# Kernel tuning notes

Measured on AMD Instinct MI355X. Metric: run time of the kernel, lower is better.

The kernel has to match this reference:

```python
import jax, jax.numpy as jnp
import numpy as np

BITWIDTH = 7
M, K, N = 32768, 1024, 1024  # tokens, in_features, out_features


def _clip8(x):
    return jnp.clip(x, -127, 127).astype(jnp.int8)


def _range_bits(x):
    # RangeEstimate: ceil(log2(max|x|)) as int, 0 if all-zero
    r = jnp.max(jnp.abs(x).astype(jnp.float32))
    bits = jnp.ceil(jnp.log2(jnp.maximum(r, 1.0)))
    return jnp.where(r == 0, 0, bits).astype(jnp.int32)


def _round_shift(x, shift):
    # RoundShift (stochastic-style bit-shift rounding); shift is a traced int32 >= 1
    p = jnp.left_shift(jnp.int32(1), shift)
    rt = jnp.floor_divide(x, p)
    prob = x - rt * p
    dec = jnp.floor_divide(prob, jnp.left_shift(jnp.int32(1), shift - 1))
    return _clip8(rt + dec)


def setup_inputs() -> dict:
    key = jax.random.key(0)
    k1, k2 = jax.random.split(key)
    act_in = jax.random.randint(k1, (M, K), -127, 128, dtype=jnp.int32).astype(jnp.int8)
    weight = jax.random.randint(k2, (N, K), -127, 128, dtype=jnp.int32).astype(jnp.int8)
    exp_in = jnp.int32(0)
    weight_exp = jnp.int32(-11)  # ceil(log2(xavier bound)) - 7 for 1024x1024
    return {"act_in": act_in, "weight": weight, "exp_in": exp_in, "weight_exp": weight_exp}


def reference(act_in, weight, exp_in, weight_exp):
    # int8 GEMM with int32 accumulation: [M,K] @ [K,N]
    acc = jnp.matmul(act_in.astype(jnp.int32), weight.T.astype(jnp.int32))
    # act_calc: range-estimate + conditional bit-shift requantize to int8
    bits = _range_bits(acc)
    shift = bits - BITWIDTH
    pos = shift > 0
    sc = jnp.maximum(shift, 1)  # safe shift for the untaken branch
    act_out = jnp.where(pos, _round_shift(acc, sc), acc.astype(jnp.int8))
    exp_out = jnp.where(pos, exp_in + weight_exp + shift, exp_in + weight_exp)
    return act_out, exp_out
```

## Files before the change

kernel.cpp:

```cpp
#include <hip/hip_runtime.h>
#include <stdint.h>


#define MM 32768
#define NN 1024
#define KK 1024
#define BM 256
#define BN 128
#define BK 64
#define NKT (KK / BK)
#define TSA (BM * BK)
#define TSB (BN * BK)

typedef __attribute__((ext_vector_type(4))) int i32x4;
typedef __attribute__((ext_vector_type(16))) int i32x16;

#define BARRIER() asm volatile("s_barrier" ::: "memory")

__device__ __forceinline__ int pack4(int a, int b, int c, int d) {
  return (int)((unsigned)(a & 0xff) | ((unsigned)(b & 0xff) << 8) |
               ((unsigned)(c & 0xff) << 16) | ((unsigned)(d & 0xff) << 24));
}

__global__ void k_init(unsigned* slot) {
  if (threadIdx.x == 0) *slot = 0u;
}

__global__ void k_pack(const int* __restrict__ src, int8_t* __restrict__ dst, int n) {
  long t = (long)blockIdx.x * blockDim.x + threadIdx.x;
  long stride = (long)gridDim.x * blockDim.x;
  for (long i = t * 16; i < (long)n; i += stride * 16) {
    const i32x4* s = (const i32x4*)(src + i);
    i32x4 a0 = s[0], a1 = s[1], a2 = s[2], a3 = s[3];
    i32x4 o;
    o[0] = pack4(a0[0], a0[1], a0[2], a0[3]);
    o[1] = pack4(a1[0], a1[1], a1[2], a1[3]);
    o[2] = pack4(a2[0], a2[1], a2[2], a2[3]);
    o[3] = pack4(a3[0], a3[1], a3[2], a3[3]);
    *(i32x4*)(dst + i) = o;
  }
}

__global__ __launch_bounds__(512, 2)
void k_gemm(const int8_t* __restrict__ A8, const int8_t* __restrict__ B8,
            int* __restrict__ out, unsigned* __restrict__ maxslot) {
  __shared__ int8_t As[3][TSA];
  __shared__ int8_t Bs[3][TSB];

  const int tid  = threadIdx.x;
  const int lane = tid & 63;
  const int w    = tid >> 6;
  const int wm   = w >> 1;
  const int wn   = w & 1;

  const int orig = blockIdx.x;
  const int wgid = ((orig & 7) << 7) + (orig >> 3);
  const int bn = wgid & 7;
  const int bm = wgid >> 3;
  const int m0 = bm * BM;
  const int n0 = bn * BN;

  i32x16 acc[2][2];
#pragma unroll
  for (int i = 0; i < 2; ++i)
#pragma unroll
    for (int j = 0; j < 2; ++j) acc[i][j] = 0;

  auto stage = [&](int buf, int kt) {
    const int k0 = kt * BK;
#pragma unroll
    for (int q = 0; q < 2; ++q) {
      const int p   = (w * 2 + q) * 1024 + lane * 16;
      const int row = p >> 6;
      const int col = (p & 63) ^ (((row >> 1) & 3) << 4);
      __builtin_amdgcn_global_load_lds(
          (const __attribute__((address_space(1))) void*)(A8 + (size_t)(m0 + row) * KK + k0 + col),
          (__attribute__((address_space(3))) void*)(&As[buf][(w * 2 + q) * 1024]),
          16, 0, 0);
    }
    {
      const int p   = w * 1024 + lane * 16;
      const int row = p >> 6;
      const int col = (p & 63) ^ (((row >> 1) & 3) << 4);
      __builtin_amdgcn_global_load_lds(
          (const __attribute__((address_space(1))) void*)(B8 + (size_t)(n0 + row) * KK + k0 + col),
          (__attribute__((address_space(3))) void*)(&Bs[buf][w * 1024]),
          16, 0, 0);
    }
  };

  auto compute = [&](int buf) {
#pragma unroll
    for (int ks = 0; ks < 2; ++ks) {
      i32x4 af[2], bf[2];
#pragma unroll
      for (int ni = 0; ni < 2; ++ni) {
        const int row = wn * 64 + ni * 32 + (lane & 31);
        const int a = row * BK +
            ((ks * 32 + ((lane >> 5) << 4)) ^ (((row >> 1) & 3) << 4));
        bf[ni] = *(const i32x4*)(&Bs[buf][a]);
      }
#pragma unroll
      for (int mi = 0; mi < 2; ++mi) {
        const int row = wm * 64 + mi * 32 + (lane & 31);
        const int a = row * BK +
            ((ks * 32 + ((lane >> 5) << 4)) ^ (((row >> 1) & 3) << 4));
        af[mi] = *(const i32x4*)(&As[buf][a]);
      }
      __builtin_amdgcn_s_setprio(1);
#pragma unroll
      for (int mi = 0; mi < 2; ++mi)
#pragma unroll
        for (int ni = 0; ni < 2; ++ni)
          acc[mi][ni] = __builtin_amdgcn_mfma_i32_32x32x32_i8(
              af[mi], bf[ni], acc[mi][ni], 0, 0, 0);
      __builtin_amdgcn_s_setprio(0);
    }
  };

  stage(0, 0);
  stage(1, 1);
  asm volatile("s_waitcnt vmcnt(3)" ::: "memory");
  BARRIER();

  int b0 = 0, b1 = 1, b2 = 2;
  for (int kt = 0; kt < NKT; ++kt) {
    const bool more2 = (kt + 2 < NKT);
    if (more2) stage(b2, kt + 2);
    compute(b0);
    if (kt + 1 < NKT) {
      if (more2) { asm volatile("s_waitcnt vmcnt(3)" ::: "memory"); }
      else       { asm volatile("s_waitcnt vmcnt(0)" ::: "memory"); }
      BARRIER();
    }
    const int t = b0; b0 = b1; b1 = b2; b2 = t;
  }

  int mx = 0;
#pragma unroll
  for (int mi = 0; mi < 2; ++mi)
#pragma unroll
    for (int ni = 0; ni < 2; ++ni)
#pragma unroll
      for (int rg = 0; rg < 16; ++rg) {
        int x = acc[mi][ni][rg];
        int a = x < 0 ? -x : x;
        mx = a > mx ? a : mx;
      }
#pragma unroll
  for (int off = 32; off >= 1; off >>= 1) {
    int o = __shfl_xor(mx, off);
    mx = o > mx ? o : mx;
  }
  if (lane == 0) atomicMax(maxslot, (unsigned)mx);

#pragma unroll
  for (int mi = 0; mi < 2; ++mi)
#pragma unroll
    for (int ni = 0; ni < 2; ++ni) {
      const int mbase = m0 + wm * 64 + mi * 32;
      const int ncol  = n0 + wn * 64 + ni * 32 + (lane & 31);
#pragma unroll
      for (int rg = 0; rg < 16; ++rg) {
        const int mrow = mbase + (rg & 3) + ((rg >> 2) << 3) + ((lane >> 5) << 2);
        out[(size_t)mrow * NN + ncol] = acc[mi][ni][rg];
      }
    }
}

__global__ __launch_bounds__(256, 2)
void k_gemm_fb(const int* __restrict__ A32, const int* __restrict__ B32,
               int* __restrict__ out, unsigned* __restrict__ maxslot) {
  __shared__ int8_t As[128 * 128];
  __shared__ int8_t Bs[128 * 128];
  const int tid = threadIdx.x, lane = tid & 63, w = tid >> 6;
  const int wr = w >> 1, wc = w & 1;
  const int bn = blockIdx.x & 7, bm = blockIdx.x >> 3;
  const int m0 = bm * 128, n0 = bn * 128;
  i32x16 acc[2][2];
#pragma unroll
  for (int i = 0; i < 2; ++i)
#pragma unroll
    for (int j = 0; j < 2; ++j) acc[i][j] = 0;
  for (int kt = 0; kt < 8; ++kt) {
    const int k0 = kt * 128;
    __syncthreads();
#pragma unroll
    for (int j = 0; j < 4; ++j) {
      const int fb = (j * 256 + tid) * 16;
      const int row = fb >> 7;
      const int swz = fb ^ ((row & 7) << 4);
      const int col = fb & 127;
      const int* sa = A32 + (size_t)(m0 + row) * KK + k0 + col;
      const int* sb = B32 + (size_t)(n0 + row) * KK + k0 + col;
      i32x4 av, bv;
#pragma unroll
      for (int t = 0; t < 4; ++t) {
        i32x4 ta = ((const i32x4*)sa)[t];
        i32x4 tb = ((const i32x4*)sb)[t];
        av[t] = pack4(ta[0], ta[1], ta[2], ta[3]);
        bv[t] = pack4(tb[0], tb[1], tb[2], tb[3]);
      }
      *(i32x4*)(As + swz) = av;
      *(i32x4*)(Bs + swz) = bv;
    }
    __syncthreads();
#pragma unroll
    for (int ks = 0; ks < 4; ++ks) {
      i32x4 af[2], bf[2];
#pragma unroll
      for (int mi = 0; mi < 2; ++mi) {
        const int row = wr * 64 + mi * 32 + (lane & 31);
        int a = row * 128 + ks * 32 + ((lane >> 5) << 4);
        a ^= (row & 7) << 4;
        af[mi] = *(const i32x4*)(As + a);
      }
#pragma unroll
      for (int ni = 0; ni < 2; ++ni) {
        const int row = wc * 64 + ni * 32 + (lane & 31);
        int a = row * 128 + ks * 32 + ((lane >> 5) << 4);
        a ^= (row & 7) << 4;
        bf[ni] = *(const i32x4*)(Bs + a);
      }
#pragma unroll
      for (int mi = 0; mi < 2; ++mi)
#pragma unroll
        for (int ni = 0; ni < 2; ++ni)
          acc[mi][ni] = __builtin_amdgcn_mfma_i32_32x32x32_i8(
              af[mi], bf[ni], acc[mi][ni], 0, 0, 0);
    }
  }
  int mx = 0;
#pragma unroll
  for (int mi = 0; mi < 2; ++mi)
#pragma unroll
    for (int ni = 0; ni < 2; ++ni)
#pragma unroll
      for (int rg = 0; rg < 16; ++rg) {
        int x = acc[mi][ni][rg];
        int a = x < 0 ? -x : x;
        mx = a > mx ? a : mx;
      }
#pragma unroll
  for (int off = 32; off >= 1; off >>= 1) {
    int o = __shfl_xor(mx, off);
    mx = o > mx ? o : mx;
  }
  if (lane == 0) atomicMax(maxslot, (unsigned)mx);
#pragma unroll
  for (int mi = 0; mi < 2; ++mi)
#pragma unroll
    for (int ni = 0; ni < 2; ++ni) {
      const int mbase = m0 + wr * 64 + mi * 32;
      const int ncol = n0 + wc * 64 + ni * 32 + (lane & 31);
#pragma unroll
      for (int rg = 0; rg < 16; ++rg) {
        const int mrow = mbase + (rg & 3) + ((rg >> 2) << 3) + ((lane >> 5) << 2);
        out[(size_t)mrow * NN + ncol] = acc[mi][ni][rg];
      }
    }
}

__global__ __launch_bounds__(256)
void k_requant(int* __restrict__ out, const unsigned* __restrict__ maxslot) {
  const unsigned r = *maxslot;
  const int bits  = (r <= 1u) ? 0 : (32 - __clz((int)(r - 1u)));
  const int shift = bits - 7;
  const size_t n = (size_t)MM * NN;
  size_t i = ((size_t)blockIdx.x * blockDim.x + threadIdx.x) * 4;
  const size_t stride = (size_t)gridDim.x * blockDim.x * 4;
  if (shift > 0) {
    for (; i < n; i += stride) {
      i32x4 v = *(i32x4*)(out + i);
#pragma unroll
      for (int j = 0; j < 4; ++j) {
        const int x = v[j];
        int t = (x >> shift) + ((x >> (shift - 1)) & 1);
        v[j] = t > 127 ? 127 : (t < -127 ? -127 : t);
      }
      *(i32x4*)(out + i) = v;
    }
  } else {
    for (; i < n; i += stride) {
      i32x4 v = *(i32x4*)(out + i);
#pragma unroll
      for (int j = 0; j < 4; ++j) v[j] = (int)(int8_t)v[j];
      *(i32x4*)(out + i) = v;
    }
  }
}

__global__ void k_final(int* __restrict__ out, const int* __restrict__ exp_in,
                        const int* __restrict__ wexp) {
  if (threadIdx.x == 0) {
    const unsigned r = *(const unsigned*)(out + (size_t)MM * NN);
    const int bits  = (r <= 1u) ? 0 : (32 - __clz((int)(r - 1u)));
    const int shift = bits - 7;
    out[(size_t)MM * NN] = *exp_in + *wexp + (shift > 0 ? shift : 0);
  }
}

extern "C" void kernel_launch(void* const* d_in, const int* in_sizes, int n_in,
                              void* d_out, int out_size, void* d_ws, size_t ws_size,
                              hipStream_t stream) {
  const int* act    = (const int*)d_in[0];
  const int* wgt    = (const int*)d_in[1];
  const int* exp_in = (const int*)d_in[2];
  const int* wexp   = (const int*)d_in[3];
  int* out          = (int*)d_out;
  unsigned* maxslot = (unsigned*)(out + (size_t)MM * NN);

  const size_t need = (size_t)(MM + NN) * KK + 256;

  k_init<<<1, 64, 0, stream>>>(maxslot);

  if (ws_size >= need) {
    int8_t* a8 = (int8_t*)d_ws;
    int8_t* w8 = a8 + (size_t)MM * KK;
    k_pack<<<2048, 256, 0, stream>>>(act, a8, MM * KK);
    k_pack<<<256, 256, 0, stream>>>(wgt, w8, NN * KK);
    const int grid = (MM / BM) * (NN / BN);
    k_gemm<<<grid, 512, 0, stream>>>(a8, w8, out, maxslot);
  } else {
    k_gemm_fb<<<(MM / 128) * (NN / 128), 256, 0, stream>>>(act, wgt, out, maxslot);
  }

  k_requant<<<4096, 256, 0, stream>>>(out, maxslot);
  k_final<<<1, 64, 0, stream>>>(out, exp_in, wexp);
}
```

Before: 195.9 us.

## Pack operands into MFMA fragment order and load directly from global

The pack kernel now writes int8 A and B in a pre-swizzled layout where each 1 KB block holds one 32x32 MFMA fragment, laid out in lane order. The GEMM then drops LDS staging, barriers and the triple buffer, and each wave loads its fragments straight from global memory with coalesced 16-byte loads. The block tile shrinks to 128x128 with 256 threads, which gives more blocks. This removes LDS traffic and sync costs, but A and B reuse now relies on L2 and there is no explicit prefetch pipeline, so global load latency may be exposed.

```diff
diff --git a/kernel.cpp b/kernel.cpp
--- a/kernel.cpp
+++ b/kernel.cpp
@@ -5,17 +5,9 @@
 #define MM 32768
 #define NN 1024
 #define KK 1024
-#define BM 256
-#define BN 128
-#define BK 64
-#define NKT (KK / BK)
-#define TSA (BM * BK)
-#define TSB (BN * BK)
 
 typedef __attribute__((ext_vector_type(4))) int i32x4;
 typedef __attribute__((ext_vector_type(16))) int i32x16;
-
-#define BARRIER() asm volatile("s_barrier" ::: "memory")
 
 __device__ __forceinline__ int pack4(int a, int b, int c, int d) {
   return (int)((unsigned)(a & 0xff) | ((unsigned)(b & 0xff) << 8) |
@@ -26,27 +18,30 @@
   if (threadIdx.x == 0) *slot = 0u;
 }
 
-__global__ void k_pack(const int* __restrict__ src, int8_t* __restrict__ dst, int n) {
-  long t = (long)blockIdx.x * blockDim.x + threadIdx.x;
-  long stride = (long)gridDim.x * blockDim.x;
-  for (long i = t * 16; i < (long)n; i += stride * 16) {
-    const i32x4* s = (const i32x4*)(src + i);
-    i32x4 a0 = s[0], a1 = s[1], a2 = s[2], a3 = s[3];
+__global__ void k_packf(const int* __restrict__ src, int8_t* __restrict__ dst,
+                        long nbytes) {
+  const long step = (long)gridDim.x * blockDim.x * 16;
+  for (long f = ((long)blockIdx.x * blockDim.x + threadIdx.x) * 16; f < nbytes;
+       f += step) {
+    const int tile = (int)(f >> 10);
+    const int lane = ((int)f >> 4) & 63;
+    const int mt = tile >> 5, kt2 = tile & 31;
+    const int row = mt * 32 + (lane & 31);
+    const int k   = kt2 * 32 + (lane >> 5) * 16;
+    const int* s = src + (size_t)row * KK + k;
     i32x4 o;
-    o[0] = pack4(a0[0], a0[1], a0[2], a0[3]);
-    o[1] = pack4(a1[0], a1[1], a1[2], a1[3]);
-    o[2] = pack4(a2[0], a2[1], a2[2], a2[3]);
-    o[3] = pack4(a3[0], a3[1], a3[2], a3[3]);
-    *(i32x4*)(dst + i) = o;
-  }
-}
-
-__global__ __launch_bounds__(512, 2)
-void k_gemm(const int8_t* __restrict__ A8, const int8_t* __restrict__ B8,
-            int* __restrict__ out, unsigned* __restrict__ maxslot) {
-  __shared__ int8_t As[3][TSA];
-  __shared__ int8_t Bs[3][TSB];
-
+#pragma unroll
+    for (int q = 0; q < 4; ++q) {
+      i32x4 t4 = ((const i32x4*)s)[q];
+      o[q] = pack4(t4[0], t4[1], t4[2], t4[3]);
+    }
+    *(i32x4*)(dst + f) = o;
+  }
+}
+
+__global__ __launch_bounds__(256)
+void k_gemmf(const int8_t* __restrict__ Af, const int8_t* __restrict__ Bf,
+             int* __restrict__ out, unsigned* __restrict__ maxslot) {
   const int tid  = threadIdx.x;
   const int lane = tid & 63;
   const int w    = tid >> 6;
@@ -54,11 +49,14 @@
   const int wn   = w & 1;
 
   const int orig = blockIdx.x;
-  const int wgid = ((orig & 7) << 7) + (orig >> 3);
+  const int wgid = ((orig & 7) << 8) + (orig >> 3);
   const int bn = wgid & 7;
   const int bm = wgid >> 3;
-  const int m0 = bm * BM;
-  const int n0 = bn * BN;
+
+  const int mtb = bm * 4 + wm * 2;
+  const int ntb = bn * 4 + wn * 2;
+  const int8_t* pa = Af + (size_t)mtb * 32 * 1024 + lane * 16;
+  const int8_t* pb = Bf + (size_t)ntb * 32 * 1024 + lane * 16;
 
   i32x16 acc[2][2];
 #pragma unroll
@@ -66,74 +64,17 @@
 #pragma unroll
     for (int j = 0; j < 2; ++j) acc[i][j] = 0;
 
-  auto stage = [&](int buf, int kt) {
-    const int k0 = kt * BK;
-#pragma unroll
-    for (int q = 0; q < 2; ++q) {
-      const int p   = (w * 2 + q) * 1024 + lane * 16;
-      const int row = p >> 6;
-      const int col = (p & 63) ^ (((row >> 1) & 3) << 4);
-      __builtin_amdgcn_global_load_lds(
-          (const __attribute__((address_space(1))) void*)(A8 + (size_t)(m0 + row) * KK + k0 + col),
-          (__attribute__((address_space(3))) void*)(&As[buf][(w * 2 + q) * 1024]),
-          16, 0, 0);
-    }
-    {
-      const int p   = w * 1024 + lane * 16;
-      const int row = p >> 6;
-      const int col = (p & 63) ^ (((row >> 1) & 3) << 4);
-      __builtin_amdgcn_global_load_lds(
-          (const __attribute__((address_space(1))) void*)(B8 + (size_t)(n0 + row) * KK + k0 + col),
-          (__attribute__((address_space(3))) void*)(&Bs[buf][w * 1024]),
-          16, 0, 0);
-    }
-  };
-
-  auto compute = [&](int buf) {
-#pragma unroll
-    for (int ks = 0; ks < 2; ++ks) {
-      i32x4 af[2], bf[2];
-#pragma unroll
-      for (int ni = 0; ni < 2; ++ni) {
-        const int row = wn * 64 + ni * 32 + (lane & 31);
-        const int a = row * BK +
-            ((ks * 32 + ((lane >> 5) << 4)) ^ (((row >> 1) & 3) << 4));
-        bf[ni] = *(const i32x4*)(&Bs[buf][a]);
-      }
-#pragma unroll
-      for (int mi = 0; mi < 2; ++mi) {
-        const int row = wm * 64 + mi * 32 + (lane & 31);
-        const int a = row * BK +
-            ((ks * 32 + ((lane >> 5) << 4)) ^ (((row >> 1) & 3) << 4));
-        af[mi] = *(const i32x4*)(&As[buf][a]);
-      }
-      __builtin_amdgcn_s_setprio(1);
-#pragma unroll
-      for (int mi = 0; mi < 2; ++mi)
-#pragma unroll
-        for (int ni = 0; ni < 2; ++ni)
-          acc[mi][ni] = __builtin_amdgcn_mfma_i32_32x32x32_i8(
-              af[mi], bf[ni], acc[mi][ni], 0, 0, 0);
-      __builtin_amdgcn_s_setprio(0);
-    }
-  };
-
-  stage(0, 0);
-  stage(1, 1);
-  asm volatile("s_waitcnt vmcnt(3)" ::: "memory");
-  BARRIER();
-
-  int b0 = 0, b1 = 1, b2 = 2;
-  for (int kt = 0; kt < NKT; ++kt) {
-    const bool more2 = (kt + 2 < NKT);
-    if (more2) stage(b2, kt + 2);
-    compute(b0);
-    if (kt + 1 < NKT) {
-      if (more2) { asm volatile("s_waitcnt vmcnt(3)" ::: "memory"); }
-      else       { asm volatile("s_waitcnt vmcnt(0)" ::: "memory"); }
-      BARRIER();
-    }
-    const int t = b0; b0 = b1; b1 = b2; b2 = t;
+#pragma unroll 4
+  for (int kt2 = 0; kt2 < 32; ++kt2) {
+    const int off = kt2 * 1024;
+    const i32x4 af0 = *(const i32x4*)(pa + off);
+    const i32x4 af1 = *(const i32x4*)(pa + 32 * 1024 + off);
+    const i32x4 bf0 = *(const i32x4*)(pb + off);
+    const i32x4 bf1 = *(const i32x4*)(pb + 32 * 1024 + off);
+    acc[0][0] = __builtin_amdgcn_mfma_i32_32x32x32_i8(af0, bf0, acc[0][0], 0, 0, 0);
+    acc[0][1] = __builtin_amdgcn_mfma_i32_32x32x32_i8(af0, bf1, acc[0][1], 0, 0, 0);
+    acc[1][0] = __builtin_amdgcn_mfma_i32_32x32x32_i8(af1, bf0, acc[1][0], 0, 0, 0);
+    acc[1][1] = __builtin_amdgcn_mfma_i32_32x32x32_i8(af1, bf1, acc[1][1], 0, 0, 0);
   }
 
   int mx = 0;
@@ -154,6 +95,8 @@
   }
   if (lane == 0) atomicMax(maxslot, (unsigned)mx);
 
+  const int m0 = bm * 128;
+  const int n0 = bn * 128;
 #pragma unroll
   for (int mi = 0; mi < 2; ++mi)
 #pragma unroll
@@ -317,10 +260,9 @@
   if (ws_size >= need) {
     int8_t* a8 = (int8_t*)d_ws;
     int8_t* w8 = a8 + (size_t)MM * KK;
-    k_pack<<<2048, 256, 0, stream>>>(act, a8, MM * KK);
-    k_pack<<<256, 256, 0, stream>>>(wgt, w8, NN * KK);
-    const int grid = (MM / BM) * (NN / BN);
-    k_gemm<<<grid, 512, 0, stream>>>(a8, w8, out, maxslot);
+    k_packf<<<4096, 256, 0, stream>>>(act, a8, (long)MM * KK);
+    k_packf<<<256, 256, 0, stream>>>(wgt, w8, (long)NN * KK);
+    k_gemmf<<<(MM / 128) * (NN / 128), 256, 0, stream>>>(a8, w8, out, maxslot);
   } else {
     k_gemm_fb<<<(MM / 128) * (NN / 128), 256, 0, stream>>>(act, wgt, out, maxslot);
   }
```

Result: slower. 201.5 us (+2.8%).
